# Performance work log

Hardware: AMD Instinct MI355X
Metric: run time of the kernel (lower is better)

Reference implementation:

```python
import jax, jax.numpy as jnp
import numpy as np

D_MODEL = 1024
D = 256
B, T = 64, 512


def setup_inputs() -> dict:
    key = jax.random.key(0)
    ks = jax.random.split(key, 7)
    s = 1.0 / np.sqrt(D_MODEL)
    return {
        "x": jax.random.normal(ks[0], (B, T, D_MODEL), dtype=jnp.float32),
        "Wq": jax.random.uniform(ks[1], (D_MODEL, D), jnp.float32, -s, s),
        "bq": jax.random.uniform(ks[2], (D,), jnp.float32, -s, s),
        "Wk": jax.random.uniform(ks[3], (D_MODEL, D), jnp.float32, -s, s),
        "bk": jax.random.uniform(ks[4], (D,), jnp.float32, -s, s),
        "Wv": jax.random.uniform(ks[5], (D_MODEL, D), jnp.float32, -s, s),
        "bv": jax.random.uniform(ks[6], (D,), jnp.float32, -s, s),
    }


def reference(x, Wq, bq, Wk, bk, Wv, bv):
    # Linear projections: [B,T,d_model] -> [B,T,d]
    q = x @ Wq + bq
    k = x @ Wk + bk
    v = x @ Wv + bv
    Tq = x.shape[1]
    scale = k.shape[-1] ** (-0.5)
    # scores: [B,T,T]
    scores = jnp.einsum('bqd,bkd->bqk', q, k) * scale
    causal = jnp.tril(jnp.ones((Tq, Tq), dtype=bool))
    scores = jnp.where(causal, scores, -jnp.inf)
    weights = jax.nn.softmax(scores, axis=-1)
    out = jnp.einsum('bqk,bkd->bqd', weights, v)
    return out
```

## Files before the change

### kernel.cpp

```cpp
#include <hip/hip_runtime.h>
#include <hip/hip_bf16.h>

typedef __attribute__((ext_vector_type(8))) short short8;
typedef __attribute__((ext_vector_type(4))) float floatx4;
typedef __attribute__((ext_vector_type(16))) float floatx16;

#define GLOAD_LDS16(src, dst) \
  __builtin_amdgcn_global_load_lds((const __attribute__((address_space(1))) unsigned int*)(src), \
      (__attribute__((address_space(3))) unsigned int*)(dst), 16, 0, 0)

__device__ __forceinline__ short f2bf(float f) {
    __hip_bfloat16 h = __float2bfloat16(f);
    return *reinterpret_cast<short*>(&h);
}

__device__ __forceinline__ floatx4 mfma16(short8 a, short8 b, floatx4 c) {
    return __builtin_amdgcn_mfma_f32_16x16x32_bf16(a, b, c, 0, 0, 0);
}

__device__ __forceinline__ floatx16 mfma32(short8 a, short8 b, floatx16 c) {
    return __builtin_amdgcn_mfma_f32_32x32x16_bf16(a, b, c, 0, 0, 0);
}

__global__ __launch_bounds__(256) void wconv_kernel(const float* __restrict__ Wq,
                                                    const float* __restrict__ Wk,
                                                    const float* __restrict__ Wv,
                                                    __hip_bfloat16* __restrict__ WT) {
    __shared__ unsigned short lds[64][65];
    const int bidx = blockIdx.x;
    const int kt = bidx & 15;
    const int ntile = bidx >> 4;
    const int gn0 = ntile * 64;
    const float* W = (gn0 < 256) ? Wq : (gn0 < 512 ? Wk : Wv);
    const int nl0 = gn0 & 255;
    const int k0 = kt * 64;
    const int tr = threadIdx.x >> 6;
    const int tc = threadIdx.x & 63;

#pragma unroll
    for (int it = 0; it < 16; ++it) {
        int r = it * 4 + tr;
        lds[r][tc] = (unsigned short)f2bf(W[(size_t)(k0 + r) * 256 + nl0 + tc]);
    }
    __syncthreads();
#pragma unroll
    for (int it = 0; it < 16; ++it) {
        int nr = it * 4 + tr;
        unsigned short u = lds[tc][nr];
        WT[(size_t)(gn0 + nr) * 1024 + k0 + tc] = *reinterpret_cast<__hip_bfloat16*>(&u);
    }
}

__global__ __launch_bounds__(512) void proj_kernel(const float* __restrict__ x,
                                                   const __hip_bfloat16* __restrict__ WT,
                                                   const float* __restrict__ bq,
                                                   const float* __restrict__ bk,
                                                   const float* __restrict__ bv,
                                                   __hip_bfloat16* __restrict__ qo,
                                                   __hip_bfloat16* __restrict__ ko,
                                                   __hip_bfloat16* __restrict__ vo) {
    __shared__ __align__(16) float As[128 * 64];
    __shared__ __align__(16) __hip_bfloat16 Bs[768 * 64];
    char* AsB = (char*)As;
    char* BsB = (char*)Bs;

    const int tid = threadIdx.x;
    const int m0 = blockIdx.x * 128;
    const int wid = tid >> 6, lane = tid & 63;
    const int wm = wid >> 2, wn = wid & 3;
    const int l31 = lane & 31, lh = lane >> 5;

    floatx16 acc[2][6];
#pragma unroll
    for (int i = 0; i < 2; ++i)
#pragma unroll
        for (int j = 0; j < 6; ++j)
#pragma unroll
            for (int e = 0; e < 16; ++e) acc[i][j][e] = 0.f;

    for (int kt = 0; kt < 16; ++kt) {
#pragma unroll
        for (int s = 0; s < 4; ++s) {
            int o = s * 8192 + tid * 16;
            int row = o >> 8;
            int sb = (o & 255) ^ ((row & 7) << 4);
            const float* src = x + (size_t)(m0 + row) * 1024 + kt * 64 + (sb >> 2);
            GLOAD_LDS16(src, AsB + o);
        }
#pragma unroll
        for (int s = 0; s < 12; ++s) {
            int o = s * 8192 + tid * 16;
            int row = o >> 7;
            int so = (o & 127) ^ ((row & 7) << 4);
            const __hip_bfloat16* src = WT + (size_t)row * 1024 + kt * 64 + (so >> 1);
            GLOAD_LDS16(src, BsB + o);
        }
        __syncthreads();

#pragma unroll
        for (int ks = 0; ks < 4; ++ks) {
            short8 af[2];
#pragma unroll
            for (int mt = 0; mt < 2; ++mt) {
                int row = wm * 64 + mt * 32 + l31;
                int rb = row * 256, msk = (row & 7) << 4;
                int b0 = ks * 64 + lh * 32;
                floatx4 f0 = *(const floatx4*)(AsB + rb + (b0 ^ msk));
                floatx4 f1 = *(const floatx4*)(AsB + rb + ((b0 + 16) ^ msk));
                short8 h;
                h[0] = f2bf(f0[0]); h[1] = f2bf(f0[1]); h[2] = f2bf(f0[2]); h[3] = f2bf(f0[3]);
                h[4] = f2bf(f1[0]); h[5] = f2bf(f1[1]); h[6] = f2bf(f1[2]); h[7] = f2bf(f1[3]);
                af[mt] = h;
            }
#pragma unroll
            for (int nt = 0; nt < 6; ++nt) {
                int row = wn * 192 + nt * 32 + l31;
                int off = ks * 32 + lh * 16;
                short8 b8 = *(const short8*)(BsB + row * 128 + (off ^ ((row & 7) << 4)));
                acc[0][nt] = mfma32(af[0], b8, acc[0][nt]);
                acc[1][nt] = mfma32(af[1], b8, acc[1][nt]);
            }
        }
        __syncthreads();
    }

#pragma unroll
    for (int nt = 0; nt < 6; ++nt) {
        int g = wn * 192 + nt * 32 + l31;
        int mat = g >> 8;
        const float* bias = (mat == 0) ? bq : (mat == 1 ? bk : bv);
        __hip_bfloat16* ob = (mat == 0) ? qo : (mat == 1 ? ko : vo);
        float scale = (mat == 0) ? 0.09016844005556021f : 1.0f;
        int c = g & 255;
        float bval = bias[c];
#pragma unroll
        for (int mt = 0; mt < 2; ++mt) {
            int base_row = m0 + wm * 64 + mt * 32 + lh * 4;
#pragma unroll
            for (int reg = 0; reg < 16; ++reg) {
                int row = base_row + (reg & 3) + 8 * (reg >> 2);
                ob[(size_t)row * 256 + c] = __float2bfloat16((acc[mt][nt][reg] + bval) * scale);
            }
        }
    }
}

__global__ __launch_bounds__(512) void attn_kernel(const __hip_bfloat16* __restrict__ q,
                                                   const __hip_bfloat16* __restrict__ k,
                                                   const __hip_bfloat16* __restrict__ v,
                                                   float* __restrict__ out) {
    __shared__ __align__(16) __hip_bfloat16 Ks[64 * 256];
    __shared__ __align__(16) __hip_bfloat16 VTs[256 * 64];
    __shared__ __align__(16) __hip_bfloat16 Ps[8][16 * 64];
    char* KsB = (char*)Ks;
    char* VTB = (char*)VTs;

    const int tid = threadIdx.x;
    const int bid = blockIdx.x;
    const int wgid = (bid & 7) * 32 + (bid >> 3);
    const int qb2 = wgid & 3, b = wgid >> 2;
    const int wid = tid >> 6, lane = tid & 63;
    const int l15 = lane & 15, lg = lane >> 4;
    char* PsB = (char*)(&Ps[wid][0]);

    short8 qf[8];
    const __hip_bfloat16* qrow = q + ((size_t)(b * 512 + qb2 * 128 + wid * 16 + l15)) * 256;
#pragma unroll
    for (int ks = 0; ks < 8; ++ks) qf[ks] = *(const short8*)(qrow + ks * 32 + lg * 8);

    float m_[4], lsum[4];
    floatx4 o[16];
#pragma unroll
    for (int r = 0; r < 4; ++r) { m_[r] = -1e30f; lsum[r] = 0.f; }
#pragma unroll
    for (int dt = 0; dt < 16; ++dt) o[dt] = (floatx4){0.f, 0.f, 0.f, 0.f};

    const int vkv = lane;
    const int vd0 = wid * 8;
    const int nchunks = qb2 * 2 + 2;
    const int qbw = qb2 * 128 + wid * 16;

    for (int c = 0; c < nchunks; ++c) {
        const size_t kvbase = (size_t)(b * 512 + c * 64) * 256;
#pragma unroll
        for (int s = 0; s < 4; ++s) {
            int o_ = s * 8192 + tid * 16;
            int row = o_ >> 9;
            int so = o_ ^ ((row & 7) << 4);
            const __hip_bfloat16* src = k + kvbase + (size_t)row * 256 + ((so & 511) >> 1);
            GLOAD_LDS16(src, KsB + o_);
        }
#pragma unroll
        for (int it = 0; it < 4; ++it) {
            int dbase = vd0 + it * 64;
            short8 vv = *(const short8*)(v + kvbase + (size_t)vkv * 256 + dbase);
#pragma unroll
            for (int j = 0; j < 8; ++j) {
                int d = dbase + j;
                int addr = (d * 128 + vkv * 2) ^ ((d & 7) << 4);
                *(short*)(VTB + addr) = vv[j];
            }
        }
        __syncthreads();

        floatx4 s4[4];
#pragma unroll
        for (int t = 0; t < 4; ++t) s4[t] = (floatx4){0.f, 0.f, 0.f, 0.f};
#pragma unroll
        for (int ks = 0; ks < 8; ++ks) {
#pragma unroll
            for (int t = 0; t < 4; ++t) {
                int kv = t * 16 + l15;
                short8 kf = *(const short8*)(KsB + kv * 512 + ((ks * 64 + lg * 16) ^ ((kv & 7) << 4)));
                s4[t] = mfma16(qf[ks], kf, s4[t]);
            }
        }
        if (c * 64 + 63 > qbw) {
#pragma unroll
            for (int t = 0; t < 4; ++t) {
                int kvg = c * 64 + t * 16 + l15;
#pragma unroll
                for (int r = 0; r < 4; ++r)
                    if (kvg > qbw + lg * 4 + r) s4[t][r] = -1e30f;
            }
        }
        float pm[4], alpha[4], rs[4];
#pragma unroll
        for (int r = 0; r < 4; ++r)
            pm[r] = fmaxf(fmaxf(s4[0][r], s4[1][r]), fmaxf(s4[2][r], s4[3][r]));
#pragma unroll
        for (int off = 1; off <= 8; off <<= 1)
#pragma unroll
            for (int r = 0; r < 4; ++r) pm[r] = fmaxf(pm[r], __shfl_xor(pm[r], off));
#pragma unroll
        for (int r = 0; r < 4; ++r) {
            float mn = fmaxf(m_[r], pm[r]);
            alpha[r] = exp2f(m_[r] - mn);
            m_[r] = mn;
        }
#pragma unroll
        for (int t = 0; t < 4; ++t)
#pragma unroll
            for (int r = 0; r < 4; ++r) s4[t][r] = exp2f(s4[t][r] - m_[r]);
#pragma unroll
        for (int r = 0; r < 4; ++r) rs[r] = s4[0][r] + s4[1][r] + s4[2][r] + s4[3][r];
#pragma unroll
        for (int off = 1; off <= 8; off <<= 1)
#pragma unroll
            for (int r = 0; r < 4; ++r) rs[r] += __shfl_xor(rs[r], off);
#pragma unroll
        for (int r = 0; r < 4; ++r) lsum[r] = lsum[r] * alpha[r] + rs[r];
#pragma unroll
        for (int dt = 0; dt < 16; ++dt) {
            o[dt][0] *= alpha[0]; o[dt][1] *= alpha[1];
            o[dt][2] *= alpha[2]; o[dt][3] *= alpha[3];
        }
#pragma unroll
        for (int t = 0; t < 4; ++t)
#pragma unroll
            for (int r = 0; r < 4; ++r) {
                int qq = lg * 4 + r;
                int addr = (qq * 128 + (t * 16 + l15) * 2) ^ ((qq & 7) << 4);
                *(short*)(PsB + addr) = f2bf(s4[t][r]);
            }
#pragma unroll
        for (int h = 0; h < 2; ++h) {
            short8 pa = *(const short8*)(PsB + l15 * 128 + ((h * 64 + lg * 16) ^ ((l15 & 7) << 4)));
#pragma unroll
            for (int dt = 0; dt < 16; ++dt) {
                int d = dt * 16 + l15;
                short8 vb = *(const short8*)(VTB + d * 128 + ((h * 64 + lg * 16) ^ ((d & 7) << 4)));
                o[dt] = mfma16(pa, vb, o[dt]);
            }
        }
        __syncthreads();
    }

    float inv[4];
#pragma unroll
    for (int r = 0; r < 4; ++r) inv[r] = 1.0f / lsum[r];
    size_t obase = ((size_t)(b * 512 + qb2 * 128 + wid * 16 + lg * 4)) * 256 + l15;
#pragma unroll
    for (int dt = 0; dt < 16; ++dt)
#pragma unroll
        for (int r = 0; r < 4; ++r)
            out[obase + (size_t)r * 256 + dt * 16] = o[dt][r] * inv[r];
}

extern "C" void kernel_launch(void* const* d_in, const int* in_sizes, int n_in,
                              void* d_out, int out_size, void* d_ws, size_t ws_size,
                              hipStream_t stream) {
    const float* x  = (const float*)d_in[0];
    const float* Wq = (const float*)d_in[1];
    const float* bq = (const float*)d_in[2];
    const float* Wk = (const float*)d_in[3];
    const float* bk = (const float*)d_in[4];
    const float* Wv = (const float*)d_in[5];
    const float* bv = (const float*)d_in[6];
    float* out = (float*)d_out;

    char* ws = (char*)d_ws;
    __hip_bfloat16* WT = (__hip_bfloat16*)ws;
    __hip_bfloat16* qo = (__hip_bfloat16*)(ws + (2u << 20));
    __hip_bfloat16* ko = qo + (size_t)32768 * 256;
    __hip_bfloat16* vo = ko + (size_t)32768 * 256;

    wconv_kernel<<<dim3(192), dim3(256), 0, stream>>>(Wq, Wk, Wv, WT);
    proj_kernel<<<dim3(256), dim3(512), 0, stream>>>(x, WT, bq, bk, bv, qo, ko, vo);
    attn_kernel<<<dim3(256), dim3(512), 0, stream>>>(qo, ko, vo, out);
}
```

Baseline: 129.1 us.

## Pre-pack weights in MFMA fragment order and halve projection K-tile

The weight conversion kernel now writes bf16 weights directly in the per-lane MFMA B-fragment layout, so the projection kernel can stream them into LDS contiguously and read each fragment with one linear 16-byte load per lane instead of swizzled addressing. The projection K-loop tile is halved from 64 to 32, doubling iterations and barriers but shrinking LDS use from 128KB to 64KB. This could allow two blocks per CU, at the cost of more synchronisation per unit of work.

```diff
diff --git a/kernel.cpp b/kernel.cpp
--- a/kernel.cpp
+++ b/kernel.cpp
@@ -22,47 +22,38 @@
     return __builtin_amdgcn_mfma_f32_32x32x16_bf16(a, b, c, 0, 0, 0);
 }
 
-__global__ __launch_bounds__(256) void wconv_kernel(const float* __restrict__ Wq,
-                                                    const float* __restrict__ Wk,
-                                                    const float* __restrict__ Wv,
-                                                    __hip_bfloat16* __restrict__ WT) {
-    __shared__ unsigned short lds[64][65];
-    const int bidx = blockIdx.x;
-    const int kt = bidx & 15;
-    const int ntile = bidx >> 4;
-    const int gn0 = ntile * 64;
-    const float* W = (gn0 < 256) ? Wq : (gn0 < 512 ? Wk : Wv);
-    const int nl0 = gn0 & 255;
-    const int k0 = kt * 64;
-    const int tr = threadIdx.x >> 6;
-    const int tc = threadIdx.x & 63;
-
-#pragma unroll
-    for (int it = 0; it < 16; ++it) {
-        int r = it * 4 + tr;
-        lds[r][tc] = (unsigned short)f2bf(W[(size_t)(k0 + r) * 256 + nl0 + tc]);
-    }
-    __syncthreads();
-#pragma unroll
-    for (int it = 0; it < 16; ++it) {
-        int nr = it * 4 + tr;
-        unsigned short u = lds[tc][nr];
-        WT[(size_t)(gn0 + nr) * 1024 + k0 + tc] = *reinterpret_cast<__hip_bfloat16*>(&u);
-    }
+__global__ __launch_bounds__(64) void wconv_kernel(const float* __restrict__ Wq,
+                                                   const float* __restrict__ Wk,
+                                                   const float* __restrict__ Wv,
+                                                   __hip_bfloat16* __restrict__ WTf) {
+    const int bid = blockIdx.x;
+    const int kb = bid / 24;
+    const int cb = bid % 24;
+    const int lane = threadIdx.x;
+    const int l31 = lane & 31, lh = lane >> 5;
+    const int n = cb * 32 + l31;
+    const float* W = (n < 256) ? Wq : (n < 512 ? Wk : Wv);
+    const int nl = n & 255;
+    const int k0 = kb * 16 + lh * 8;
+
+    short8 h;
+#pragma unroll
+    for (int j = 0; j < 8; ++j)
+        h[j] = f2bf(W[(size_t)(k0 + j) * 256 + nl]);
+    *(short8*)((char*)WTf + (size_t)bid * 1024 + lane * 16) = h;
 }
 
 __global__ __launch_bounds__(512) void proj_kernel(const float* __restrict__ x,
-                                                   const __hip_bfloat16* __restrict__ WT,
+                                                   const __hip_bfloat16* __restrict__ WTf,
                                                    const float* __restrict__ bq,
                                                    const float* __restrict__ bk,
                                                    const float* __restrict__ bv,
                                                    __hip_bfloat16* __restrict__ qo,
                                                    __hip_bfloat16* __restrict__ ko,
                                                    __hip_bfloat16* __restrict__ vo) {
-    __shared__ __align__(16) float As[128 * 64];
-    __shared__ __align__(16) __hip_bfloat16 Bs[768 * 64];
-    char* AsB = (char*)As;
-    char* BsB = (char*)Bs;
+    __shared__ __align__(16) char Ab[16384];
+    __shared__ __align__(16) char Bb[49152];
+    const char* WfB = (const char*)WTf;
 
     const int tid = threadIdx.x;
     const int m0 = blockIdx.x * 128;
@@ -78,35 +69,32 @@
 #pragma unroll
             for (int e = 0; e < 16; ++e) acc[i][j][e] = 0.f;
 
-    for (int kt = 0; kt < 16; ++kt) {
-#pragma unroll
-        for (int s = 0; s < 4; ++s) {
-            int o = s * 8192 + tid * 16;
-            int row = o >> 8;
-            int sb = (o & 255) ^ ((row & 7) << 4);
-            const float* src = x + (size_t)(m0 + row) * 1024 + kt * 64 + (sb >> 2);
-            GLOAD_LDS16(src, AsB + o);
-        }
-#pragma unroll
-        for (int s = 0; s < 12; ++s) {
+    for (int kt = 0; kt < 32; ++kt) {
+#pragma unroll
+        for (int s = 0; s < 2; ++s) {
             int o = s * 8192 + tid * 16;
             int row = o >> 7;
-            int so = (o & 127) ^ ((row & 7) << 4);
-            const __hip_bfloat16* src = WT + (size_t)row * 1024 + kt * 64 + (so >> 1);
-            GLOAD_LDS16(src, BsB + o);
-        }
-        __syncthreads();
-
-#pragma unroll
-        for (int ks = 0; ks < 4; ++ks) {
+            int sb = (o & 127) ^ ((row & 7) << 4);
+            const float* src = x + (size_t)(m0 + row) * 1024 + kt * 32 + (sb >> 2);
+            GLOAD_LDS16(src, Ab + o);
+        }
+#pragma unroll
+        for (int s = 0; s < 6; ++s) {
+            int o = s * 8192 + tid * 16;
+            GLOAD_LDS16(WfB + (((size_t)kt * 48) << 10) + o, Bb + o);
+        }
+        __syncthreads();
+
+#pragma unroll
+        for (int ks = 0; ks < 2; ++ks) {
             short8 af[2];
 #pragma unroll
             for (int mt = 0; mt < 2; ++mt) {
                 int row = wm * 64 + mt * 32 + l31;
-                int rb = row * 256, msk = (row & 7) << 4;
+                int rb = row * 128, msk = (row & 7) << 4;
                 int b0 = ks * 64 + lh * 32;
-                floatx4 f0 = *(const floatx4*)(AsB + rb + (b0 ^ msk));
-                floatx4 f1 = *(const floatx4*)(AsB + rb + ((b0 + 16) ^ msk));
+                floatx4 f0 = *(const floatx4*)(Ab + rb + (b0 ^ msk));
+                floatx4 f1 = *(const floatx4*)(Ab + rb + ((b0 + 16) ^ msk));
                 short8 h;
                 h[0] = f2bf(f0[0]); h[1] = f2bf(f0[1]); h[2] = f2bf(f0[2]); h[3] = f2bf(f0[3]);
                 h[4] = f2bf(f1[0]); h[5] = f2bf(f1[1]); h[6] = f2bf(f1[2]); h[7] = f2bf(f1[3]);
@@ -114,9 +102,8 @@
             }
 #pragma unroll
             for (int nt = 0; nt < 6; ++nt) {
-                int row = wn * 192 + nt * 32 + l31;
-                int off = ks * 32 + lh * 16;
-                short8 b8 = *(const short8*)(BsB + row * 128 + (off ^ ((row & 7) << 4)));
+                int f = ks * 24 + wn * 6 + nt;
+                short8 b8 = *(const short8*)(Bb + (f << 10) + lane * 16);
                 acc[0][nt] = mfma32(af[0], b8, acc[0][nt]);
                 acc[1][nt] = mfma32(af[1], b8, acc[1][nt]);
             }
@@ -300,12 +287,12 @@
     float* out = (float*)d_out;
 
     char* ws = (char*)d_ws;
-    __hip_bfloat16* WT = (__hip_bfloat16*)ws;
+    __hip_bfloat16* WTf = (__hip_bfloat16*)ws;
     __hip_bfloat16* qo = (__hip_bfloat16*)(ws + (2u << 20));
     __hip_bfloat16* ko = qo + (size_t)32768 * 256;
     __hip_bfloat16* vo = ko + (size_t)32768 * 256;
 
-    wconv_kernel<<<dim3(192), dim3(256), 0, stream>>>(Wq, Wk, Wv, WT);
-    proj_kernel<<<dim3(256), dim3(512), 0, stream>>>(x, WT, bq, bk, bv, qo, ko, vo);
+    wconv_kernel<<<dim3(1536), dim3(64), 0, stream>>>(Wq, Wk, Wv, WTf);
+    proj_kernel<<<dim3(256), dim3(512), 0, stream>>>(x, WTf, bq, bk, bv, qo, ko, vo);
     attn_kernel<<<dim3(256), dim3(512), 0, stream>>>(qo, ko, vo, out);
 }
```

New measurement: 130.2 us. No clear change (+0.8%).
